# Optimization experiments

Hardware: AMD Instinct MI355X
Metric: run time of the kernel (lower is better)

Reference implementation:

```python
import jax, jax.numpy as jnp
import numpy as np

B, N, M = 64, 1025, 1024          # N = M + 1 (node 0 is the zero-padding node)
TREE_FEAT = 96
QVEC = 95                          # sum(range(10)) + 10*5
IN_CH = TREE_FEAT + 32             # tree features + q_conv output
EPS = 1e-5


def _tree_conv(x, idx, W, b):
    # x: (B, C, N); idx: (B, 3M) child-triple indices into node axis
    g = jnp.take_along_axis(x, idx[:, None, :], axis=2)        # (B, C, 3M)
    Bn, C, L = g.shape
    g = g.reshape(Bn, C, L // 3, 3)                            # (B, C, M, 3)
    out = jnp.einsum('bcmk,ock->bom', g, W) + b[None, :, None] # Conv1d k=3 s=3
    zero = jnp.zeros((Bn, W.shape[0], 1), out.dtype)           # re-prepend zero node
    return jnp.concatenate([zero, out], axis=2)                # (B, O, M+1)


def _tree_norm(x):
    # TreeLayerNorm: per-sample mean/std over (channels, nodes); torch.std is unbiased
    mean = jnp.mean(x, axis=(1, 2), keepdims=True)
    std = jnp.std(x, axis=(1, 2), keepdims=True, ddof=1)
    return (x - mean) / (std + EPS)


def setup_inputs() -> dict:
    key = jax.random.key(0)
    ks = jax.random.split(key, 17)
    p = lambda k, s: jax.random.normal(k, s, dtype=jnp.float32) * 0.05
    return {
        'q_vecs': jax.random.normal(ks[0], (B, QVEC), dtype=jnp.float32),
        'trees': jax.random.normal(ks[1], (B, N, TREE_FEAT), dtype=jnp.float32),
        'idxes': jax.random.randint(ks[2], (B, 3 * M), 0, N),
        # q_conv: Linear(95,64) -> Linear(64,128) -> Linear(128,64) -> Linear(64,32)
        'Wq1': p(ks[3], (QVEC, 64)),  'bq1': jnp.zeros((64,), jnp.float32),
        'Wq2': p(ks[4], (64, 128)),   'bq2': jnp.zeros((128,), jnp.float32),
        'Wq3': p(ks[5], (128, 64)),   'bq3': jnp.zeros((64,), jnp.float32),
        'Wq4': p(ks[6], (64, 32)),    'bq4': jnp.zeros((32,), jnp.float32),
        # tree_conv kernels: (out, in, 3)
        'Wc1': p(ks[7], (512, IN_CH, 3)), 'bc1': jnp.zeros((512,), jnp.float32),
        'Wc2': p(ks[8], (256, 512, 3)),   'bc2': jnp.zeros((256,), jnp.float32),
        'Wc3': p(ks[9], (128, 256, 3)),   'bc3': jnp.zeros((128,), jnp.float32),
    }


def reference(q_vecs, trees, idxes,
              Wq1, bq1, Wq2, bq2, Wq3, bq3, Wq4, bq4,
              Wc1, bc1, Wc2, bc2, Wc3, bc3):
    # q_conv: 4 stacked linears (no nonlinearity between them in the source)
    q = q_vecs @ Wq1 + bq1
    q = q @ Wq2 + bq2
    q = q @ Wq3 + bq3
    q = q @ Wq4 + bq4                                    # (B, 32)

    Bn, Nn = trees.shape[:2]
    q_rep = jnp.broadcast_to(q[:, None, :], (Bn, Nn, q.shape[-1]))
    aug = jnp.concatenate([trees, q_rep], axis=2)        # (B, N, IN_CH)
    x = jnp.transpose(aug, (0, 2, 1))                    # (B, IN_CH, N)

    x = _tree_conv(x, idxes, Wc1, bc1)
    x = jax.nn.leaky_relu(_tree_norm(x), negative_slope=0.01)
    x = _tree_conv(x, idxes, Wc2, bc2)
    x = jax.nn.leaky_relu(_tree_norm(x), negative_slope=0.01)
    x = _tree_conv(x, idxes, Wc3, bc3)
    x = _tree_norm(x)
    return jnp.max(x, axis=2)                            # DynamicPooling -> (B, 128)
```

## Files before the change

### kernel.cpp

```cpp
#include <hip/hip_runtime.h>
#include <hip/hip_bf16.h>

typedef __attribute__((ext_vector_type(8))) short short8;
typedef __attribute__((ext_vector_type(4))) float f32x4;

#define EPSV 1e-5f

__device__ __forceinline__ float bf2f(ushort u){
  union { uint i; float f; } x; x.i = ((uint)u) << 16; return x.f;
}
__device__ __forceinline__ ushort f2bf(float f){
  union { float f; uint i; } x; x.f = f;
  uint r = (x.i + 0x7FFFu + ((x.i >> 16) & 1u)) >> 16;
  return (ushort)r;
}

__global__ void init_kernel(ushort* x1, float* stats, int* maxbuf){
  int i = blockIdx.x * 256 + threadIdx.x;
  if (i < 384)  stats[i] = 0.f;
  if (i < 8192) maxbuf[i] = 0;
  if (i < 32768){ int b = i >> 9, c = i & 511; x1[(size_t)b*1025*512 + c] = 0; }
}

__global__ void zero2_kernel(ushort* x2){
  int i = blockIdx.x * 256 + threadIdx.x;
  int b = i >> 8, c = i & 255;
  x2[(size_t)b*1025*256 + c] = 0;
}

__global__ void qconv_kernel(const float* __restrict__ qv,
    const float* __restrict__ W1, const float* __restrict__ b1,
    const float* __restrict__ W2, const float* __restrict__ b2,
    const float* __restrict__ W3, const float* __restrict__ b3,
    const float* __restrict__ W4, const float* __restrict__ b4,
    float* __restrict__ qout){
  __shared__ float v0[96], h1[64], h2[128], h3[64];
  int b = blockIdx.x, t = threadIdx.x;
  if (t < 95) v0[t] = qv[b*95 + t];
  __syncthreads();
  if (t < 64){ float s = b1[t]; for (int i=0;i<95;i++)  s += v0[i]*W1[i*64 + t];  h1[t]=s; }
  __syncthreads();
  if (t < 128){ float s = b2[t]; for (int i=0;i<64;i++)  s += h1[i]*W2[i*128 + t]; h2[t]=s; }
  __syncthreads();
  if (t < 64){ float s = b3[t]; for (int i=0;i<128;i++) s += h2[i]*W3[i*64 + t];  h3[t]=s; }
  __syncthreads();
  if (t < 32){ float s = b4[t]; for (int i=0;i<64;i++)  s += h3[i]*W4[i*32 + t];  qout[b*32 + t]=s; }
}

__global__ void aug_kernel(const float* __restrict__ trees, const float* __restrict__ q,
                           ushort* __restrict__ aug){
  int n = blockIdx.x;
  int b = blockIdx.y;
  int c = threadIdx.x;
  float v = (c < 96) ? trees[((size_t)b*1025 + n)*96 + c] : q[b*32 + (c - 96)];
  aug[(((size_t)b*1025 + n) << 7) + c] = f2bf(v);
}

__global__ void prepw_kernel(const float* __restrict__ wc, ushort* __restrict__ wt,
                             int O, int C){
  int i = blockIdx.x * 256 + threadIdx.x;
  int total = O * 3 * C;
  if (i >= total) return;
  int o  = i / (3*C);
  int K  = i - o*3*C;
  int kp = K / C;
  int c  = K - kp*C;
  wt[i] = f2bf(wc[(o*C + c)*3 + kp]);
}

template<int CIN, bool DO_MAX>
__global__ __launch_bounds__(256) void conv_kernel(
    const ushort* __restrict__ xin, const ushort* __restrict__ wt,
    const float* __restrict__ bias, const int* __restrict__ idxes,
    ushort* __restrict__ xout, float* __restrict__ stats, int* __restrict__ maxbuf){
  constexpr int K3 = 3 * CIN;
  constexpr int NT = K3 / 32;
  const int COUT = gridDim.y * 128;
  const int b  = blockIdx.z;
  const int m0 = blockIdx.x * 128;
  const int o0 = blockIdx.y * 128;
  const int t  = threadIdx.x;
  const int lane = t & 63, wid = t >> 6;
  const int WM = (wid & 1) * 64, WO = (wid >> 1) * 64;
  const int fr = lane & 15, fg = lane >> 4;

  __shared__ __align__(16) union {
    struct { ushort A[2][128][40]; ushort B[2][128][40]; } s;
    ushort stage[128][132];
  } sh;
  __shared__ int idx_s[384];

  for (int i = t; i < 384; i += 256) idx_s[i] = idxes[b*3072 + m0*3 + i];
  __syncthreads();

  const ushort* xb = xin + (size_t)b * 1025 * CIN;
  const int rr = t >> 1, cb = (t & 1) * 16;

  uint4 ra0, ra1, rb0, rb1;
  auto GLOAD = [&](int ch){
    int k0 = ch * 32;
    int kp = k0 / CIN;
    int c  = k0 - kp * CIN;
    int node = idx_s[rr*3 + kp];
    const ushort* sa = xb + (size_t)node * CIN + c + cb;
    ra0 = *reinterpret_cast<const uint4*>(sa);
    ra1 = *reinterpret_cast<const uint4*>(sa + 8);
    const ushort* sb = wt + (size_t)(o0 + rr) * K3 + k0 + cb;
    rb0 = *reinterpret_cast<const uint4*>(sb);
    rb1 = *reinterpret_cast<const uint4*>(sb + 8);
  };
  auto DSW = [&](int bf){
    *reinterpret_cast<uint4*>(&sh.s.A[bf][rr][cb])     = ra0;
    *reinterpret_cast<uint4*>(&sh.s.A[bf][rr][cb + 8]) = ra1;
    *reinterpret_cast<uint4*>(&sh.s.B[bf][rr][cb])     = rb0;
    *reinterpret_cast<uint4*>(&sh.s.B[bf][rr][cb + 8]) = rb1;
  };

  f32x4 acc[4][4] = {};

  GLOAD(0);
  DSW(0);
  __syncthreads();
  int cur = 0;
  for (int ch = 0; ch < NT; ++ch){
    if (ch + 1 < NT) GLOAD(ch + 1);
    short8 af[4], bfr[4];
    #pragma unroll
    for (int i = 0; i < 4; ++i){
      af[i]  = *reinterpret_cast<const short8*>(&sh.s.A[cur][WM + i*16 + fr][fg*8]);
      bfr[i] = *reinterpret_cast<const short8*>(&sh.s.B[cur][WO + i*16 + fr][fg*8]);
    }
    #pragma unroll
    for (int mf = 0; mf < 4; ++mf)
      #pragma unroll
      for (int nf = 0; nf < 4; ++nf)
        acc[mf][nf] = __builtin_amdgcn_mfma_f32_16x16x32_bf16(af[mf], bfr[nf], acc[mf][nf], 0, 0, 0);
    if (ch + 1 < NT){
      DSW(cur ^ 1);
      __syncthreads();
      cur ^= 1;
    }
  }

  float bsv[4];
  #pragma unroll
  for (int nf = 0; nf < 4; ++nf) bsv[nf] = bias[o0 + WO + nf*16 + fr];
  float lsum = 0.f, lsq = 0.f;
  float cmax[4] = { -1e30f, -1e30f, -1e30f, -1e30f };
  #pragma unroll
  for (int mf = 0; mf < 4; ++mf)
    #pragma unroll
    for (int nf = 0; nf < 4; ++nf)
      #pragma unroll
      for (int i = 0; i < 4; ++i){
        float v = acc[mf][nf][i] + bsv[nf];
        lsum += v; lsq += v*v;
        if (DO_MAX) cmax[nf] = fmaxf(cmax[nf], v);
        else acc[mf][nf][i] = v;
      }
  #pragma unroll
  for (int off = 1; off < 64; off <<= 1){
    lsum += __shfl_xor(lsum, off);
    lsq  += __shfl_xor(lsq,  off);
  }
  if (lane == 0){
    atomicAdd(&stats[b],      lsum);
    atomicAdd(&stats[64 + b], lsq);
  }
  if (DO_MAX){
    #pragma unroll
    for (int nf = 0; nf < 4; ++nf){
      float v = cmax[nf];
      v = fmaxf(v, __shfl_xor(v, 16));
      v = fmaxf(v, __shfl_xor(v, 32));
      if (lane < 16)
        atomicMax(&maxbuf[b*COUT + o0 + WO + nf*16 + fr], __float_as_int(v));
    }
  } else {
    __syncthreads();
    #pragma unroll
    for (int mf = 0; mf < 4; ++mf)
      #pragma unroll
      for (int nf = 0; nf < 4; ++nf)
        #pragma unroll
        for (int i = 0; i < 4; ++i)
          sh.stage[WM + mf*16 + fg*4 + i][WO + nf*16 + fr] = f2bf(acc[mf][nf][i]);
    __syncthreads();
    #pragma unroll
    for (int it = 0; it < 16; ++it){
      int row = it*8 + (t >> 5);
      int col = (t & 31) * 4;
      uint2 v = *reinterpret_cast<const uint2*>(&sh.stage[row][col]);
      *reinterpret_cast<uint2*>(xout + ((size_t)(b*1025 + 1 + m0 + row))*COUT + o0 + col) = v;
    }
  }
}

__global__ void norm_kernel(ushort* __restrict__ x, const float* __restrict__ st,
                            float cnt, int nvec_per_b){
  int b = blockIdx.y;
  int j = blockIdx.x * 256 + threadIdx.x;
  if (j >= nvec_per_b) return;
  float sum = st[b], sq = st[64 + b];
  float mean = sum / cnt;
  float var  = fmaxf((sq - sum*sum/cnt) / (cnt - 1.f), 0.f);
  float rs   = 1.f / (sqrtf(var) + EPSV);
  ushort* p = x + ((size_t)b * nvec_per_b + j) * 8;
  union { uint4 v; ushort u[8]; } d;
  d.v = *reinterpret_cast<const uint4*>(p);
  #pragma unroll
  for (int k = 0; k < 8; ++k){
    float f = bf2f(d.u[k]);
    f = (f - mean) * rs;
    f = (f >= 0.f) ? f : 0.01f * f;
    d.u[k] = f2bf(f);
  }
  *reinterpret_cast<uint4*>(p) = d.v;
}

__global__ void final_kernel(const int* __restrict__ maxbuf, const float* __restrict__ st,
                             float* __restrict__ out){
  int i = blockIdx.x * 256 + threadIdx.x;
  int b = i >> 7;
  const float cnt = 131200.f;
  float sum = st[b], sq = st[64 + b];
  float mean = sum / cnt;
  float var  = fmaxf((sq - sum*sum/cnt) / (cnt - 1.f), 0.f);
  float rs   = 1.f / (sqrtf(var) + EPSV);
  out[i] = (__int_as_float(maxbuf[i]) - mean) * rs;
}

static constexpr size_t SZ_X1  = (size_t)64*1025*512*2;
static constexpr size_t SZ_X2  = (size_t)64*1025*256*2;
static constexpr size_t OFF_X1 = 0;
static constexpr size_t OFF_X2 = OFF_X1 + SZ_X1;
static constexpr size_t OFF_AUG = OFF_X2;
static constexpr size_t OFF_WT1 = OFF_X2 + SZ_X2;
static constexpr size_t OFF_WT2 = OFF_WT1 + (size_t)512*384*2;
static constexpr size_t OFF_WT3 = OFF_WT2 + (size_t)256*1536*2;
static constexpr size_t OFF_Q   = OFF_WT3 + (size_t)128*768*2;
static constexpr size_t OFF_ST  = OFF_Q + (size_t)64*32*4;
static constexpr size_t OFF_MAX = OFF_ST + (size_t)384*4;

extern "C" void kernel_launch(void* const* d_in, const int* in_sizes, int n_in,
                              void* d_out, int out_size, void* d_ws, size_t ws_size,
                              hipStream_t stream){
  const float* q_vecs = (const float*)d_in[0];
  const float* trees  = (const float*)d_in[1];
  const int*   idxes  = (const int*)  d_in[2];
  const float* Wq1 = (const float*)d_in[3];  const float* bq1 = (const float*)d_in[4];
  const float* Wq2 = (const float*)d_in[5];  const float* bq2 = (const float*)d_in[6];
  const float* Wq3 = (const float*)d_in[7];  const float* bq3 = (const float*)d_in[8];
  const float* Wq4 = (const float*)d_in[9];  const float* bq4 = (const float*)d_in[10];
  const float* Wc1 = (const float*)d_in[11]; const float* bc1 = (const float*)d_in[12];
  const float* Wc2 = (const float*)d_in[13]; const float* bc2 = (const float*)d_in[14];
  const float* Wc3 = (const float*)d_in[15]; const float* bc3 = (const float*)d_in[16];
  float* out = (float*)d_out;
  char* ws = (char*)d_ws;

  ushort* x1    = (ushort*)(ws + OFF_X1);
  ushort* x2    = (ushort*)(ws + OFF_X2);
  ushort* aug   = (ushort*)(ws + OFF_AUG);
  ushort* wt1   = (ushort*)(ws + OFF_WT1);
  ushort* wt2   = (ushort*)(ws + OFF_WT2);
  ushort* wt3   = (ushort*)(ws + OFF_WT3);
  float*  qbuf  = (float*) (ws + OFF_Q);
  float*  stats = (float*) (ws + OFF_ST);
  int*    maxb  = (int*)   (ws + OFF_MAX);

  init_kernel<<<128, 256, 0, stream>>>(x1, stats, maxb);
  qconv_kernel<<<64, 128, 0, stream>>>(q_vecs, Wq1,bq1, Wq2,bq2, Wq3,bq3, Wq4,bq4, qbuf);
  aug_kernel<<<dim3(1025, 64), 128, 0, stream>>>(trees, qbuf, aug);
  prepw_kernel<<<(512*384 + 255)/256, 256, 0, stream>>>(Wc1, wt1, 512, 128);
  prepw_kernel<<<(256*1536 + 255)/256, 256, 0, stream>>>(Wc2, wt2, 256, 512);
  prepw_kernel<<<(128*768 + 255)/256, 256, 0, stream>>>(Wc3, wt3, 128, 256);

  conv_kernel<128, false><<<dim3(8, 4, 64), 256, 0, stream>>>(aug, wt1, bc1, idxes, x1, stats +   0, nullptr);
  zero2_kernel<<<64, 256, 0, stream>>>(x2);
  norm_kernel<<<dim3((65600 + 255)/256, 64), 256, 0, stream>>>(x1, stats +   0, 524800.f, 65600);
  conv_kernel<512, false><<<dim3(8, 2, 64), 256, 0, stream>>>(x1,  wt2, bc2, idxes, x2, stats + 128, nullptr);
  norm_kernel<<<dim3((32800 + 255)/256, 64), 256, 0, stream>>>(x2, stats + 128, 262400.f, 32800);
  conv_kernel<256, true ><<<dim3(8, 1, 64), 256, 0, stream>>>(x2,  wt3, bc3, idxes, nullptr, stats + 256, maxb);
  final_kernel<<<32, 256, 0, stream>>>(maxb, stats + 256, out);
}
```

Measured before the change: 318.5 us.

## Use direct global-to-LDS loads with triple-buffered pipeline and XCD-aware block remap

Replaces the register-staged double-buffered gather with global_load_lds direct-to-LDS copies into a three-stage ring, waiting on vmcnt instead of a full sync after each LDS write. The LDS tiles lose their row padding and use an XOR swizzle of column chunks to limit bank conflicts. Blocks are launched on a 1D grid and remapped so consecutive work units land on the same XCD, improving L2 locality of shared weights and batch rows. MFMA sections also raise wave priority. This adds reliance on precise vmcnt accounting and the ordering of the swizzle against the LDS write layout.

```diff
diff --git a/kernel.cpp b/kernel.cpp
--- a/kernel.cpp
+++ b/kernel.cpp
@@ -13,6 +13,12 @@
   union { float f; uint i; } x; x.f = f;
   uint r = (x.i + 0x7FFFu + ((x.i >> 16) & 1u)) >> 16;
   return (ushort)r;
+}
+
+__device__ __forceinline__ void gl_lds16(const void* g, void* l){
+  __builtin_amdgcn_global_load_lds(
+      (const __attribute__((address_space(1))) unsigned int*)g,
+      (__attribute__((address_space(3))) unsigned int*)l, 16, 0, 0);
 }
 
 __global__ void init_kernel(ushort* x1, float* stats, int* maxbuf){
@@ -68,24 +74,30 @@
   wt[i] = f2bf(wc[(o*C + c)*3 + kp]);
 }
 
-template<int CIN, bool DO_MAX>
+template<int CIN, int GY, bool DO_MAX>
 __global__ __launch_bounds__(256) void conv_kernel(
     const ushort* __restrict__ xin, const ushort* __restrict__ wt,
     const float* __restrict__ bias, const int* __restrict__ idxes,
     ushort* __restrict__ xout, float* __restrict__ stats, int* __restrict__ maxbuf){
-  constexpr int K3 = 3 * CIN;
-  constexpr int NT = K3 / 32;
-  const int COUT = gridDim.y * 128;
-  const int b  = blockIdx.z;
-  const int m0 = blockIdx.x * 128;
-  const int o0 = blockIdx.y * 128;
-  const int t  = threadIdx.x;
+  constexpr int K3   = 3 * CIN;
+  constexpr int NT   = K3 / 32;
+  constexpr int COUT = GY * 128;
+  constexpr int NWG  = 8 * GY * 64;
+
+  const int bid = blockIdx.x;
+  const int wu  = (bid & 7) * (NWG >> 3) + (bid >> 3);
+  const int m0  = (wu & 7) * 128;
+  const int rest = wu >> 3;
+  const int o0  = (rest % GY) * 128;
+  const int b   = rest / GY;
+
+  const int t = threadIdx.x;
   const int lane = t & 63, wid = t >> 6;
   const int WM = (wid & 1) * 64, WO = (wid >> 1) * 64;
   const int fr = lane & 15, fg = lane >> 4;
 
   __shared__ __align__(16) union {
-    struct { ushort A[2][128][40]; ushort B[2][128][40]; } s;
+    struct { ushort A[3][128][32]; ushort B[3][128][32]; } s;
     ushort stage[128][132];
   } sh;
   __shared__ int idx_s[384];
@@ -94,52 +106,52 @@
   __syncthreads();
 
   const ushort* xb = xin + (size_t)b * 1025 * CIN;
-  const int rr = t >> 1, cb = (t & 1) * 16;
-
-  uint4 ra0, ra1, rb0, rb1;
-  auto GLOAD = [&](int ch){
-    int k0 = ch * 32;
-    int kp = k0 / CIN;
-    int c  = k0 - kp * CIN;
-    int node = idx_s[rr*3 + kp];
-    const ushort* sa = xb + (size_t)node * CIN + c + cb;
-    ra0 = *reinterpret_cast<const uint4*>(sa);
-    ra1 = *reinterpret_cast<const uint4*>(sa + 8);
-    const ushort* sb = wt + (size_t)(o0 + rr) * K3 + k0 + cb;
-    rb0 = *reinterpret_cast<const uint4*>(sb);
-    rb1 = *reinterpret_cast<const uint4*>(sb + 8);
+  const int w16  = wid * 16;
+  const int row0 = w16 + (lane >> 2);
+  const int row1 = 64 + row0;
+  const int coff = ((lane & 3) ^ ((lane >> 3) & 3)) * 8;
+  const int n00 = idx_s[row0*3 + 0], n01 = idx_s[row0*3 + 1], n02 = idx_s[row0*3 + 2];
+  const int n10 = idx_s[row1*3 + 0], n11 = idx_s[row1*3 + 1], n12 = idx_s[row1*3 + 2];
+  const ushort* wtb0 = wt + (size_t)(o0 + row0) * K3 + coff;
+  const ushort* wtb1 = wt + (size_t)(o0 + row1) * K3 + coff;
+
+  auto ISSUE = [&](int ch, int bf){
+    const int k0 = ch * 32;
+    const int kp = k0 / CIN;
+    const int c0 = k0 - kp * CIN;
+    const int a0 = (kp == 0) ? n00 : (kp == 1) ? n01 : n02;
+    const int a1 = (kp == 0) ? n10 : (kp == 1) ? n11 : n12;
+    gl_lds16(xb + (size_t)a0 * CIN + c0 + coff, &sh.s.A[bf][w16][0]);
+    gl_lds16(xb + (size_t)a1 * CIN + c0 + coff, &sh.s.A[bf][64 + w16][0]);
+    gl_lds16(wtb0 + k0, &sh.s.B[bf][w16][0]);
+    gl_lds16(wtb1 + k0, &sh.s.B[bf][64 + w16][0]);
   };
-  auto DSW = [&](int bf){
-    *reinterpret_cast<uint4*>(&sh.s.A[bf][rr][cb])     = ra0;
-    *reinterpret_cast<uint4*>(&sh.s.A[bf][rr][cb + 8]) = ra1;
-    *reinterpret_cast<uint4*>(&sh.s.B[bf][rr][cb])     = rb0;
-    *reinterpret_cast<uint4*>(&sh.s.B[bf][rr][cb + 8]) = rb1;
-  };
 
   f32x4 acc[4][4] = {};
-
-  GLOAD(0);
-  DSW(0);
-  __syncthreads();
-  int cur = 0;
+  const int fc = (fg ^ ((fr >> 1) & 3)) * 8;
+
+  ISSUE(0, 0);
+  ISSUE(1, 1);
+
   for (int ch = 0; ch < NT; ++ch){
-    if (ch + 1 < NT) GLOAD(ch + 1);
-    short8 af[4], bfr[4];
+    if (ch < NT - 1) asm volatile("s_waitcnt vmcnt(4)" ::: "memory");
+    else             asm volatile("s_waitcnt vmcnt(0)" ::: "memory");
+    __builtin_amdgcn_s_barrier();
+    if (ch + 2 < NT) ISSUE(ch + 2, (ch + 2) % 3);
+    const int cur = ch % 3;
+    short8 af[4], bf4[4];
     #pragma unroll
     for (int i = 0; i < 4; ++i){
-      af[i]  = *reinterpret_cast<const short8*>(&sh.s.A[cur][WM + i*16 + fr][fg*8]);
-      bfr[i] = *reinterpret_cast<const short8*>(&sh.s.B[cur][WO + i*16 + fr][fg*8]);
+      af[i]  = *reinterpret_cast<const short8*>(&sh.s.A[cur][WM + i*16 + fr][fc]);
+      bf4[i] = *reinterpret_cast<const short8*>(&sh.s.B[cur][WO + i*16 + fr][fc]);
     }
+    __builtin_amdgcn_s_setprio(1);
     #pragma unroll
     for (int mf = 0; mf < 4; ++mf)
       #pragma unroll
       for (int nf = 0; nf < 4; ++nf)
-        acc[mf][nf] = __builtin_amdgcn_mfma_f32_16x16x32_bf16(af[mf], bfr[nf], acc[mf][nf], 0, 0, 0);
-    if (ch + 1 < NT){
-      DSW(cur ^ 1);
-      __syncthreads();
-      cur ^= 1;
-    }
+        acc[mf][nf] = __builtin_amdgcn_mfma_f32_16x16x32_bf16(af[mf], bf4[nf], acc[mf][nf], 0, 0, 0);
+    __builtin_amdgcn_s_setprio(0);
   }
 
   float bsv[4];
@@ -275,11 +287,11 @@
   prepw_kernel<<<(256*1536 + 255)/256, 256, 0, stream>>>(Wc2, wt2, 256, 512);
   prepw_kernel<<<(128*768 + 255)/256, 256, 0, stream>>>(Wc3, wt3, 128, 256);
 
-  conv_kernel<128, false><<<dim3(8, 4, 64), 256, 0, stream>>>(aug, wt1, bc1, idxes, x1, stats +   0, nullptr);
+  conv_kernel<128, 4, false><<<2048, 256, 0, stream>>>(aug, wt1, bc1, idxes, x1, stats +   0, nullptr);
   zero2_kernel<<<64, 256, 0, stream>>>(x2);
   norm_kernel<<<dim3((65600 + 255)/256, 64), 256, 0, stream>>>(x1, stats +   0, 524800.f, 65600);
-  conv_kernel<512, false><<<dim3(8, 2, 64), 256, 0, stream>>>(x1,  wt2, bc2, idxes, x2, stats + 128, nullptr);
+  conv_kernel<512, 2, false><<<1024, 256, 0, stream>>>(x1,  wt2, bc2, idxes, x2, stats + 128, nullptr);
   norm_kernel<<<dim3((32800 + 255)/256, 64), 256, 0, stream>>>(x2, stats + 128, 262400.f, 32800);
-  conv_kernel<256, true ><<<dim3(8, 1, 64), 256, 0, stream>>>(x2,  wt3, bc3, idxes, nullptr, stats + 256, maxb);
+  conv_kernel<256, 1, true ><<<512, 256, 0, stream>>>(x2,  wt3, bc3, idxes, nullptr, stats + 256, maxb);
   final_kernel<<<32, 256, 0, stream>>>(maxb, stats + 256, out);
 }
```

Result: slower. 325.7 us (+2.3%).
